# Kernel tuning notes

Measured on AMD Instinct MI355X. Metric: run time of the kernel, lower is better.

## Reference

```python
import jax, jax.numpy as jnp
import numpy as np

HEAD_DIM = 128
N_HEADS = 32
ROPE_DIM = 64
TOPK = 1024
B, S, HID, QLORA = 1, 2048, 4096, 1536
LN_EPS = 1e-5  # torch nn.LayerNorm default


def _hadamard_matrix(n):
    H = np.array([[1.0]], dtype=np.float32)
    while H.shape[0] < n:
        H = np.block([[H, H], [H, -H]])
    return jnp.asarray(H)

_H128 = _hadamard_matrix(HEAD_DIM)
_FWHT_SCALE = HEAD_DIM ** -0.5


def rotate_activation(x):
    # Fast Walsh-Hadamard transform == x @ H_sylvester, scaled by dim**-0.5
    return (x @ _H128) * _FWHT_SCALE


def rope_non_interleaved(x, cos, sin):
    # x: [..., rope_dim]; cos/sin: broadcastable [..., rope_dim/2]
    half = x.shape[-1] // 2
    x1, x2 = x[..., :half], x[..., half:]
    return jnp.concatenate([x1 * cos - x2 * sin, x1 * sin + x2 * cos], axis=-1)


def setup_inputs() -> dict:
    key = jax.random.key(0)
    ks = jax.random.split(key, 8)
    hidden_states = jax.random.normal(ks[0], (B, S, HID), jnp.float32)
    q_compressed = jax.random.normal(ks[1], (B, S, QLORA), jnp.float32)
    # rotary cos/sin for rope_dim=64 (standard concat layout)
    pos = jnp.arange(S, dtype=jnp.float32)
    inv_freq = 1.0 / (10000.0 ** (jnp.arange(0, ROPE_DIM, 2, dtype=jnp.float32) / ROPE_DIM))
    ang = pos[:, None] * inv_freq[None, :]  # [S, 32]
    cos = jnp.tile(jnp.cos(ang), (1, 2))[None]  # [1, S, 64]
    sin = jnp.tile(jnp.sin(ang), (1, 2))[None]
    # additive causal mask [B, S, S]
    causal = jnp.tril(jnp.ones((S, S), jnp.bool_))
    attention_mask = jnp.where(causal, 0.0, -1e9).astype(jnp.float32)[None]
    Wq_b = jax.random.normal(ks[2], (QLORA, N_HEADS * HEAD_DIM), jnp.float32) * (QLORA ** -0.5)
    Wk = jax.random.normal(ks[3], (HID, HEAD_DIM), jnp.float32) * (HID ** -0.5)
    k_gamma = jnp.ones((HEAD_DIM,), jnp.float32)
    k_beta = jnp.zeros((HEAD_DIM,), jnp.float32)
    Ww = jax.random.normal(ks[4], (HID, N_HEADS), jnp.float32) * (HID ** -0.5)
    return {"hidden_states": hidden_states, "q_compressed": q_compressed, "cos": cos,
            "sin": sin, "attention_mask": attention_mask, "Wq_b": Wq_b, "Wk": Wk,
            "k_gamma": k_gamma, "k_beta": k_beta, "Ww": Ww}


def reference(hidden_states, q_compressed, cos, sin, attention_mask, Wq_b, Wk, k_gamma, k_beta, Ww):
    b, s, _ = hidden_states.shape
    softmax_scale = HEAD_DIM ** -0.5
    # queries: [b, s, H, D]
    q = (q_compressed @ Wq_b).reshape(b, s, N_HEADS, HEAD_DIM)
    q_rope, q_nope = q[..., :ROPE_DIM], q[..., ROPE_DIM:]
    # keys: single shared head, LayerNorm(k)
    k = hidden_states @ Wk  # [b, s, D]
    mu = jnp.mean(k, axis=-1, keepdims=True)
    var = jnp.mean(jnp.square(k - mu), axis=-1, keepdims=True)
    k = (k - mu) * jax.lax.rsqrt(var + LN_EPS) * k_gamma + k_beta
    k_rope, k_nope = k[..., :ROPE_DIM], k[..., ROPE_DIM:]
    # non-interleaved RoPE (cos/sin truncated to half_dim=32)
    half = ROPE_DIM // 2
    c, sn = cos[..., :half], sin[..., :half]
    q_rope = rope_non_interleaved(q_rope, c[:, :, None, :], sn[:, :, None, :])
    k_rope = rope_non_interleaved(k_rope, c, sn)
    q = jnp.concatenate([q_rope, q_nope], axis=-1)
    k = jnp.concatenate([k_rope, k_nope], axis=-1)
    # Hadamard activation rotation
    q = rotate_activation(q)
    k = rotate_activation(k)
    # I_{t,s} = sum_h w_{t,h} * ReLU(q_{t,h} . k_s) * scale
    scores = jax.nn.relu(jnp.einsum('bthd,bsd->bths', q, k)) * softmax_scale
    weights = hidden_states @ Ww  # [b, t, H]
    index_scores = jnp.einsum('bths,bth->bts', scores, weights)
    index_scores = index_scores + attention_mask
    topk = min(TOPK, s)
    _, topk_indices = jax.lax.top_k(index_scores, topk)  # [b, s, topk]
    return topk_indices, index_scores
```

## Files before the change

### kernel.cpp

```cpp
#include <hip/hip_runtime.h>
#include <stdint.h>

#define S_LEN 2048
#define HID 4096
#define QLORA 1536
#define NH 32
#define HD 128
#define TOPK_N 1024
#define NEG_INF -1000000000.0f
#define INV_SQRT_HD 0.08838834764831844f

typedef __attribute__((ext_vector_type(8))) short short8;
typedef __attribute__((ext_vector_type(4))) short short4_;
typedef __attribute__((ext_vector_type(4))) float float4_;
typedef __attribute__((ext_vector_type(4))) unsigned uint4_;
typedef __attribute__((ext_vector_type(4))) int int4_;
typedef __attribute__((ext_vector_type(2))) int int2_;

__device__ __forceinline__ short f2bf(float x) {
  union { float f; unsigned u; } v; v.f = x;
  unsigned r = v.u + 0x7FFFu + ((v.u >> 16) & 1u);
  return (short)(r >> 16);
}

__device__ __forceinline__ unsigned f2ord(float x) {
  union { float f; unsigned u; } v; v.f = x;
  return v.u ^ (0x80000000u | (unsigned)((int)v.u >> 31));
}

__device__ __forceinline__ void gload_lds16(const void* g, void* l) {
  __builtin_amdgcn_global_load_lds((const __attribute__((address_space(1))) unsigned int*)g,
                                   (__attribute__((address_space(3))) unsigned int*)l, 16, 0, 0);
}

__global__ __launch_bounds__(256) void prep_kernel(
    const float* __restrict__ hidden, short* __restrict__ hidb,
    const float* __restrict__ qc, char* __restrict__ qc8,
    float* __restrict__ kacc,
    const float* __restrict__ wqb, char* __restrict__ wq8T,
    const float* __restrict__ wk, const float* __restrict__ ww,
    short* __restrict__ kwT) {
  __shared__ __align__(8) char stile[4352];
  int bid = blockIdx.x;
  const int tid = threadIdx.x;
  if (bid < 8192) {
    int i = bid * 256 + tid;
    float4 v = ((const float4*)hidden)[i];
    short4_ o;
    o[0] = f2bf(v.x); o[1] = f2bf(v.y); o[2] = f2bf(v.z); o[3] = f2bf(v.w);
    ((short4_*)hidb)[i] = o;
    return;
  }
  if (bid < 9728) {
    int i = (bid - 8192) * 256 + tid;
    float4 f0 = ((const float4*)qc)[i * 2];
    float4 f1 = ((const float4*)qc)[i * 2 + 1];
    int lo = 0, hi = 0;
    lo = __builtin_amdgcn_cvt_pk_fp8_f32(f0.x, f0.y, lo, 0);
    lo = __builtin_amdgcn_cvt_pk_fp8_f32(f0.z, f0.w, lo, 1);
    hi = __builtin_amdgcn_cvt_pk_fp8_f32(f1.x, f1.y, hi, 0);
    hi = __builtin_amdgcn_cvt_pk_fp8_f32(f1.z, f1.w, hi, 1);
    ((int2_*)qc8)[i] = (int2_){lo, hi};
    return;
  }
  if (bid < 10048) {
    int i = (bid - 9728) * 256 + tid;
    ((float4_*)kacc)[i] = (float4_){0.f, 0.f, 0.f, 0.f};
    return;
  }
  if (bid < 13120) {
    char (*t8)[33] = (char(*)[33])stile;
    int b = bid - 10048;
    int k0 = (b >> 7) * 64, n0 = (b & 127) * 32;
    #pragma unroll
    for (int i = 0; i < 8; i++) {
      int e = tid + i * 256;
      int r = e >> 5, c = e & 31;
      float x = wqb[(size_t)(k0 + r) * HID + n0 + c];
      t8[r][c] = (char)__builtin_amdgcn_cvt_pk_fp8_f32(x, x, 0, 0);
    }
    __syncthreads();
    int nl = tid >> 3, jk = (tid & 7) * 8;
    union { char c[8]; long l; } o;
    #pragma unroll
    for (int j = 0; j < 8; j++) o.c[j] = t8[jk + j][nl];
    *(long*)(wq8T + (size_t)(n0 + nl) * QLORA + k0 + jk) = o.l;
    return;
  }
  short (*tile)[33] = (short(*)[33])stile;
  const float* in; short* out; int R, C, bx, by;
  if (bid < 13632) {
    int b2 = bid - 13120;
    in = wk; out = kwT; R = HID; C = HD; bx = b2 & 3; by = b2 >> 2;
  } else {
    int b3 = bid - 13632;
    in = ww; out = kwT + 128 * HID; R = HID; C = NH; bx = 0; by = b3;
  }
  int c0 = bx * 32, r0 = by * 32;
  int tx = tid & 31, ty = tid >> 5;
  #pragma unroll
  for (int i = 0; i < 32; i += 8)
    tile[ty + i][tx] = f2bf(in[(size_t)(r0 + ty + i) * C + c0 + tx]);
  __syncthreads();
  #pragma unroll
  for (int i = 0; i < 32; i += 8)
    out[(size_t)(c0 + ty + i) * R + r0 + tx] = tile[tx][ty + i];
}

#define QSTAGE8(kt, Ad, Bd) do { \
  _Pragma("unroll") \
  for (int i = 0; i < 4; i++) { \
    int m = w * 32 + i * 8 + lr; \
    int gb = (kt) * 128 + ((lc ^ (m & 7)) << 4); \
    gload_lds16(qc8 + (size_t)(t0 + m) * QLORA + gb, (Ad) + (w * 32 + i * 8) * 128); \
    gload_lds16(wq8T + (size_t)(n0 + m) * QLORA + gb, (Bd) + (w * 32 + i * 8) * 128); \
  } \
} while (0)

#define QCOMPUTE8(Aq, Bq) do { \
  _Pragma("unroll") \
  for (int p = 0; p < 4; p++) { \
    int ch = p * 2 + (quad >> 1); \
    int lo8 = (quad & 1) * 8; \
    long a[2], b[8]; \
    _Pragma("unroll") \
    for (int mt = 0; mt < 2; mt++) { \
      int m = w * 32 + mt * 16 + l15; \
      a[mt] = *(const long*)((Aq) + m * 128 + ((ch ^ (m & 7)) << 4) + lo8); \
    } \
    _Pragma("unroll") \
    for (int nt = 0; nt < 8; nt++) { \
      int n = nt * 16 + l15; \
      b[nt] = *(const long*)((Bq) + n * 128 + ((ch ^ (n & 7)) << 4) + lo8); \
    } \
    _Pragma("unroll") \
    for (int mt = 0; mt < 2; mt++) \
      _Pragma("unroll") \
      for (int nt = 0; nt < 8; nt++) \
        acc[mt][nt] = __builtin_amdgcn_mfma_f32_16x16x32_fp8_fp8(a[mt], b[nt], acc[mt][nt], 0, 0, 0); \
  } \
} while (0)

__global__ __launch_bounds__(256, 2) void gemms_kernel(
    const char* __restrict__ qc8, const char* __restrict__ wq8T,
    const float* __restrict__ cosp, const float* __restrict__ sinp,
    short* __restrict__ qrot,
    const short* __restrict__ hidb, const short* __restrict__ kwT,
    float* __restrict__ kacc) {
  __shared__ __align__(16) char smem[65536];
  const int tid = threadIdx.x;
  const int w = tid >> 6, lane = tid & 63;
  const int l15 = lane & 15, quad = lane >> 4;
  const int lr = lane >> 3, lc = lane & 7;

  if (blockIdx.x < 512) {
    char* A0 = smem;
    char* B0 = smem + 16384;
    char* A1 = smem + 32768;
    char* B1 = smem + 49152;
    const int n0 = (blockIdx.x & 31) * 128;
    const int t0 = (blockIdx.x >> 5) * 128;

    float4_ acc[2][8];
    #pragma unroll
    for (int mt = 0; mt < 2; mt++)
      #pragma unroll
      for (int i = 0; i < 8; i++) acc[mt][i] = (float4_){0.f, 0.f, 0.f, 0.f};

    QSTAGE8(0, A0, B0);
    __syncthreads();
    for (int kt = 0; kt < 12; kt += 2) {
      QSTAGE8(kt + 1, A1, B1);
      QCOMPUTE8(A0, B0);
      __syncthreads();
      if (kt + 2 < 12) QSTAGE8(kt + 2, A0, B0);
      QCOMPUTE8(A1, B1);
      __syncthreads();
    }

    #pragma unroll
    for (int mt = 0; mt < 2; mt++) {
      #pragma unroll
      for (int r = 0; r < 4; r++) {
        const int trow = t0 + w * 32 + mt * 16 + quad * 4 + r;
        float v[8];
        #pragma unroll
        for (int nt = 0; nt < 8; nt++) v[nt] = acc[mt][nt][r];
        float cc0 = cosp[trow * 64 + l15], cc1 = cosp[trow * 64 + 16 + l15];
        float ss0 = sinp[trow * 64 + l15], ss1 = sinp[trow * 64 + 16 + l15];
        float r0 = v[0] * cc0 - v[2] * ss0, r1 = v[1] * cc1 - v[3] * ss1;
        float r2 = v[0] * ss0 + v[2] * cc0, r3 = v[1] * ss1 + v[3] * cc1;
        v[0] = r0; v[1] = r1; v[2] = r2; v[3] = r3;
        short* orow = qrot + (size_t)trow * HID + n0;
        #pragma unroll
        for (int nt = 0; nt < 8; nt++)
          orow[nt * 16 + l15] = f2bf(v[nt]);
      }
    }
  } else {
    short* Al = (short*)smem;
    short* Bl = (short*)(smem + 8192);
    const int b2 = blockIdx.x - 512;
    const int kc0 = (b2 & 7) * 512;
    const int m0g = (b2 >> 3) * 64;

    float4_ acc[10];
    #pragma unroll
    for (int i = 0; i < 10; i++) acc[i] = (float4_){0.f, 0.f, 0.f, 0.f};

    for (int k0 = kc0; k0 < kc0 + 512; k0 += 64) {
      #pragma unroll
      for (int i = 0; i < 2; i++) {
        int m = w * 16 + i * 8 + lr;
        int gk = k0 + ((lc ^ (m & 7)) << 3);
        gload_lds16(hidb + (size_t)(m0g + m) * HID + gk, Al + (w * 16 + i * 8) * 64);
      }
      #pragma unroll
      for (int i = 0; i < 5; i++) {
        int n = w * 40 + i * 8 + lr;
        int gk = k0 + ((lc ^ (n & 7)) << 3);
        gload_lds16(kwT + (size_t)n * HID + gk, Bl + (w * 40 + i * 8) * 64);
      }
      __syncthreads();
      #pragma unroll
      for (int kk = 0; kk < 64; kk += 32) {
        int ca = (kk >> 3) + quad;
        int ma = w * 16 + l15;
        short8 a = *(const short8*)(Al + ma * 64 + ((ca ^ (ma & 7)) << 3));
        #pragma unroll
        for (int nt = 0; nt < 10; nt++) {
          int n = nt * 16 + l15;
          short8 b = *(const short8*)(Bl + n * 64 + ((ca ^ (n & 7)) << 3));
          acc[nt] = __builtin_amdgcn_mfma_f32_16x16x32_bf16(a, b, acc[nt], 0, 0, 0);
        }
      }
      __syncthreads();
    }
    #pragma unroll
    for (int nt = 0; nt < 10; nt++)
      #pragma unroll
      for (int r = 0; r < 4; r++) {
        int row = m0g + w * 16 + quad * 4 + r;
        atomicAdd(&kacc[(size_t)row * 160 + nt * 16 + l15], acc[nt][r]);
      }
  }
}

__global__ __launch_bounds__(256) void ln_rope_kernel(
    const float* __restrict__ kacc, const float* __restrict__ gamma,
    const float* __restrict__ beta, const float* __restrict__ cosp,
    const float* __restrict__ sinp, short* __restrict__ krot) {
  const int tid = threadIdx.x;
  const int row = blockIdx.x * 16 + (tid >> 4);
  const int l16 = tid & 15;
  const int c0 = l16 * 8;
  const float* rp = kacc + (size_t)row * 160 + c0;
  float4 f0 = ((const float4*)rp)[0], f1 = ((const float4*)rp)[1];
  float v[8] = {f0.x, f0.y, f0.z, f0.w, f1.x, f1.y, f1.z, f1.w};
  float s = 0.f, ss = 0.f;
  #pragma unroll
  for (int j = 0; j < 8; j++) { s += v[j]; ss += v[j] * v[j]; }
  #pragma unroll
  for (int d = 1; d <= 8; d <<= 1) {
    s += __shfl_xor(s, d, 64); ss += __shfl_xor(ss, d, 64);
  }
  float mu = s * (1.0f / 128.0f);
  float var = ss * (1.0f / 128.0f) - mu * mu;
  float rs = rsqrtf(var + 1e-5f);
  #pragma unroll
  for (int j = 0; j < 8; j++)
    v[j] = (v[j] - mu) * rs * gamma[c0 + j] + beta[c0 + j];
  #pragma unroll
  for (int j = 0; j < 8; j++) {
    float p = __shfl_xor(v[j], 4, 64);
    if (l16 < 8) {
      int idx = (c0 + j) & 31;
      float c = cosp[row * 64 + idx], sn = sinp[row * 64 + idx];
      v[j] = v[j] * c + p * ((l16 < 4) ? -sn : sn);
    }
  }
  short8 o;
  #pragma unroll
  for (int j = 0; j < 8; j++) o[j] = f2bf(v[j]);
  *(short8*)(krot + (size_t)row * 128 + c0) = o;
}

__global__ __launch_bounds__(256, 2) void scores_kernel(
    const short* __restrict__ qrot, const short* __restrict__ krot,
    const float* __restrict__ kacc, float* __restrict__ isc) {
  __shared__ __align__(16) char smem[65536];
  short* buf0 = (short*)smem;
  short* buf1 = (short*)(smem + 32768);

  const int tid = threadIdx.x;
  const int w = tid >> 6, lane = tid & 63;
  const int l15 = lane & 15, quad = lane >> 4;
  const int wm = w >> 1, wn = w & 1;
  const int lr16 = lane >> 4, lc16 = lane & 15;

  const int bid = blockIdx.x;
  const int strip = (bid & 1) ? (511 - (bid >> 1)) : (bid >> 1);
  const int t0 = strip * 4;
  const int nsb = (t0 + 3) / 128 + 1;

  const short* Abase = qrot + (size_t)t0 * 32 * 128;
  #pragma unroll
  for (int i = 0; i < 8; i++) {
    int m = (w * 8 + i) * 4 + lr16;
    int gofs = m * 128 + ((lc16 ^ (m & 7)) << 3);
    gload_lds16(Abase + gofs, buf0 + (w * 8 + i) * 512);
    gload_lds16(krot + gofs, buf1 + (w * 8 + i) * 512);
  }
  __syncthreads();

  short8 af[4][4];
  #pragma unroll
  for (int k4 = 0; k4 < 4; k4++) {
    int ca = k4 * 4 + quad;
    #pragma unroll
    for (int mt = 0; mt < 4; mt++) {
      int m = wm * 64 + mt * 16 + l15;
      af[k4][mt] = *(const short8*)(buf0 + m * 128 + ((ca ^ (m & 7)) << 3));
    }
  }

  const int t_a = t0 + wm * 2, t_b = t_a + 1;
  float wq[4][4];
  #pragma unroll
  for (int mt = 0; mt < 4; mt++) {
    int tt = (mt < 2) ? t_a : t_b;
    #pragma unroll
    for (int r = 0; r < 4; r++)
      wq[mt][r] = kacc[(size_t)tt * 160 + 128 + (mt & 1) * 16 + quad * 4 + r];
  }
  __syncthreads();

  for (int sb = 0; sb < nsb; sb++) {
    short* cur = (sb & 1) ? buf0 : buf1;
    if (sb + 1 < nsb) {
      short* nxt = (sb & 1) ? buf1 : buf0;
      const short* Bbase = krot + (size_t)(sb + 1) * 128 * 128;
      #pragma unroll
      for (int i = 0; i < 8; i++) {
        int m = (w * 8 + i) * 4 + lr16;
        int gofs = m * 128 + ((lc16 ^ (m & 7)) << 3);
        gload_lds16(Bbase + gofs, nxt + (w * 8 + i) * 512);
      }
    }

    float4_ acc[4][4];
    #pragma unroll
    for (int mt = 0; mt < 4; mt++)
      #pragma unroll
      for (int nt = 0; nt < 4; nt++) acc[mt][nt] = (float4_){0.f, 0.f, 0.f, 0.f};

    #pragma unroll
    for (int k4 = 0; k4 < 4; k4++) {
      int ca = k4 * 4 + quad;
      short8 b[4];
      #pragma unroll
      for (int nt = 0; nt < 4; nt++) {
        int n = wn * 64 + nt * 16 + l15;
        b[nt] = *(const short8*)(cur + n * 128 + ((ca ^ (n & 7)) << 3));
      }
      #pragma unroll
      for (int mt = 0; mt < 4; mt++)
        #pragma unroll
        for (int nt = 0; nt < 4; nt++)
          acc[mt][nt] = __builtin_amdgcn_mfma_f32_16x16x32_bf16(af[k4][mt], b[nt], acc[mt][nt], 0, 0, 0);
    }

    #pragma unroll
    for (int nt = 0; nt < 4; nt++) {
      float pa = 0.f, pb = 0.f;
      #pragma unroll
      for (int r = 0; r < 4; r++) {
        pa += fmaxf(acc[0][nt][r], 0.f) * wq[0][r] + fmaxf(acc[1][nt][r], 0.f) * wq[1][r];
        pb += fmaxf(acc[2][nt][r], 0.f) * wq[2][r] + fmaxf(acc[3][nt][r], 0.f) * wq[3][r];
      }
      pa += __shfl_xor(pa, 16, 64); pa += __shfl_xor(pa, 32, 64);
      pb += __shfl_xor(pb, 16, 64); pb += __shfl_xor(pb, 32, 64);
      int s = sb * 128 + wn * 64 + nt * 16 + l15;
      if (quad == 0)
        isc[(size_t)t_a * S_LEN + s] = (s <= t_a) ? pa * INV_SQRT_HD : NEG_INF;
      else if (quad == 1)
        isc[(size_t)t_b * S_LEN + s] = (s <= t_b) ? pb * INV_SQRT_HD : NEG_INF;
    }

    __syncthreads();
  }

  if (wn == 0) {
    const int myrow = (lane < 32) ? t_a : t_b;
    const int l32 = lane & 31;
    float4_ nf = (float4_){NEG_INF, NEG_INF, NEG_INF, NEG_INF};
    float4_* rowp = (float4_*)(isc + (size_t)myrow * S_LEN);
    for (int i = nsb * 32 + l32; i < 512; i += 32) rowp[i] = nf;
  }
}

#define CEK(x, y, d) { if ((d) ? (v[x] < v[y]) : (v[x] > v[y])) { unsigned _t = v[x]; v[x] = v[y]; v[y] = _t; } }

__device__ __forceinline__ void shfl_phase(unsigned v[8], int j, int base, bool d) {
  const int delta = j >> 3;
  const bool keep_max = (((base & j) == 0) == d);
  #pragma unroll
  for (int r = 0; r < 8; r++) {
    unsigned pv = (unsigned)__shfl_xor((int)v[r], delta, 64);
    unsigned mx = v[r] > pv ? v[r] : pv;
    unsigned mn = v[r] > pv ? pv : v[r];
    v[r] = keep_max ? mx : mn;
  }
}

__device__ __forceinline__ void reg_phase(unsigned v[8], bool d) {
  CEK(0, 4, d); CEK(1, 5, d); CEK(2, 6, d); CEK(3, 7, d);
  CEK(0, 2, d); CEK(1, 3, d); CEK(4, 6, d); CEK(5, 7, d);
  CEK(0, 1, d); CEK(2, 3, d); CEK(4, 5, d); CEK(6, 7, d);
}

__device__ __forceinline__ int chswz(int c) { return c ^ ((c >> 3) & 7); }

__device__ __forceinline__ void lds_phase(unsigned v[8], unsigned* keys, int tid, int base,
                                          int j, bool d) {
  const int c0 = tid * 2, c1 = c0 + 1;
  ((uint4_*)keys)[chswz(c0)] = (uint4_){v[0], v[1], v[2], v[3]};
  ((uint4_*)keys)[chswz(c1)] = (uint4_){v[4], v[5], v[6], v[7]};
  __syncthreads();
  const int ptid = tid ^ (j >> 3);
  uint4_ u0 = ((uint4_*)keys)[chswz(ptid * 2)];
  uint4_ u1 = ((uint4_*)keys)[chswz(ptid * 2 + 1)];
  unsigned p[8] = {u0[0], u0[1], u0[2], u0[3], u1[0], u1[1], u1[2], u1[3]};
  const bool keep_max = (((base & j) == 0) == d);
  #pragma unroll
  for (int r = 0; r < 8; r++) {
    unsigned mx = v[r] > p[r] ? v[r] : p[r];
    unsigned mn = v[r] > p[r] ? p[r] : v[r];
    v[r] = keep_max ? mx : mn;
  }
  __syncthreads();
}

__global__ __launch_bounds__(256) void topk_kernel(const float* __restrict__ isc,
                                                   int* __restrict__ idx_out) {
  __shared__ __align__(16) unsigned keys[2048];
  const int t = blockIdx.x;
  const int tid = threadIdx.x;
  const int base = tid * 8;
  unsigned v[8];
  {
    const float* row = isc + (size_t)t * S_LEN;
    float4 f0 = ((const float4*)row)[tid * 2];
    float4 f1 = ((const float4*)row)[tid * 2 + 1];
    v[0] = (f2ord(f0.x) & 0xFFFFF800u) | (unsigned)(2047 - base - 0);
    v[1] = (f2ord(f0.y) & 0xFFFFF800u) | (unsigned)(2047 - base - 1);
    v[2] = (f2ord(f0.z) & 0xFFFFF800u) | (unsigned)(2047 - base - 2);
    v[3] = (f2ord(f0.w) & 0xFFFFF800u) | (unsigned)(2047 - base - 3);
    v[4] = (f2ord(f1.x) & 0xFFFFF800u) | (unsigned)(2047 - base - 4);
    v[5] = (f2ord(f1.y) & 0xFFFFF800u) | (unsigned)(2047 - base - 5);
    v[6] = (f2ord(f1.z) & 0xFFFFF800u) | (unsigned)(2047 - base - 6);
    v[7] = (f2ord(f1.w) & 0xFFFFF800u) | (unsigned)(2047 - base - 7);
  }
  CEK(0, 1, true); CEK(2, 3, false); CEK(4, 5, true); CEK(6, 7, false);
  CEK(0, 2, true); CEK(1, 3, true); CEK(4, 6, false); CEK(5, 7, false);
  CEK(0, 1, true); CEK(2, 3, true); CEK(4, 5, false); CEK(6, 7, false);
  {
    bool d8 = ((base & 8) == 0);
    CEK(0, 4, d8); CEK(1, 5, d8); CEK(2, 6, d8); CEK(3, 7, d8);
    CEK(0, 2, d8); CEK(1, 3, d8); CEK(4, 6, d8); CEK(5, 7, d8);
    CEK(0, 1, d8); CEK(2, 3, d8); CEK(4, 5, d8); CEK(6, 7, d8);
  }
  #pragma unroll
  for (int kb = 4; kb <= 11; kb++) {
    const int k = 1 << kb;
    const bool d = ((base & k) == 0);
    for (int j = k >> 1; j >= 512; j >>= 1)
      lds_phase(v, keys, tid, base, j, d);
    {
      int jtop = (k >> 1) < 256 ? (k >> 1) : 256;
      for (int j = jtop; j >= 8; j >>= 1)
        shfl_phase(v, j, base, d);
    }
    reg_phase(v, d);
  }
  if (tid < 128) {
    int4_ o0, o1;
    #pragma unroll
    for (int r = 0; r < 4; r++) o0[r] = 2047 - (int)(v[r] & 0x7FFu);
    #pragma unroll
    for (int r = 0; r < 4; r++) o1[r] = 2047 - (int)(v[4 + r] & 0x7FFu);
    ((int4_*)(idx_out + (size_t)t * TOPK_N))[tid * 2] = o0;
    ((int4_*)(idx_out + (size_t)t * TOPK_N))[tid * 2 + 1] = o1;
  }
}

extern "C" void kernel_launch(void* const* d_in, const int* in_sizes, int n_in,
                              void* d_out, int out_size, void* d_ws, size_t ws_size,
                              hipStream_t stream) {
  const float* hidden = (const float*)d_in[0];
  const float* qc     = (const float*)d_in[1];
  const float* cosp   = (const float*)d_in[2];
  const float* sinp   = (const float*)d_in[3];
  const float* wqb    = (const float*)d_in[5];
  const float* wk     = (const float*)d_in[6];
  const float* gamma  = (const float*)d_in[7];
  const float* beta   = (const float*)d_in[8];
  const float* ww     = (const float*)d_in[9];

  char* ws = (char*)d_ws;
  short* hidb = (short*)ws;
  char*  qc8  = (char*)(ws + 16777216);
  char*  wq8T = (char*)(ws + 19922944);
  short* kwT  = (short*)(ws + 26214400);
  short* krot = (short*)(ws + 27525120);
  short* qrot = (short*)(ws + 28049408);
  float* kacc = (float*)(ws + 44826624);

  int*   idx_out = (int*)d_out;
  float* isc     = ((float*)d_out) + (size_t)S_LEN * TOPK_N;

  prep_kernel<<<dim3(13760), dim3(256), 0, stream>>>(hidden, hidb, qc, qc8, kacc,
                                                     wqb, wq8T, wk, ww, kwT);
  gemms_kernel<<<dim3(768), dim3(256), 0, stream>>>(qc8, wq8T, cosp, sinp, qrot,
                                                    hidb, kwT, kacc);
  ln_rope_kernel<<<dim3(128), dim3(256), 0, stream>>>(kacc, gamma, beta, cosp, sinp, krot);
  scores_kernel<<<dim3(512), dim3(256), 0, stream>>>(qrot, krot, kacc, isc);
  topk_kernel<<<dim3(2048), dim3(256), 0, stream>>>(isc, idx_out);
}
```

Before: 246.1 us.

## Sort each top-k row within one wavefront using register bitonic networks

New measurement: 228.9 us. 7.0% less time.

```diff
diff --git a/kernel.cpp b/kernel.cpp
--- a/kernel.cpp
+++ b/kernel.cpp
@@ -399,98 +399,152 @@
   }
 }
 
-#define CEK(x, y, d) { if ((d) ? (v[x] < v[y]) : (v[x] > v[y])) { unsigned _t = v[x]; v[x] = v[y]; v[y] = _t; } }
-
-__device__ __forceinline__ void shfl_phase(unsigned v[8], int j, int base, bool d) {
-  const int delta = j >> 3;
-  const bool keep_max = (((base & j) == 0) == d);
-  #pragma unroll
-  for (int r = 0; r < 8; r++) {
-    unsigned pv = (unsigned)__shfl_xor((int)v[r], delta, 64);
-    unsigned mx = v[r] > pv ? v[r] : pv;
-    unsigned mn = v[r] > pv ? pv : v[r];
-    v[r] = keep_max ? mx : mn;
-  }
-}
-
-__device__ __forceinline__ void reg_phase(unsigned v[8], bool d) {
-  CEK(0, 4, d); CEK(1, 5, d); CEK(2, 6, d); CEK(3, 7, d);
-  CEK(0, 2, d); CEK(1, 3, d); CEK(4, 6, d); CEK(5, 7, d);
-  CEK(0, 1, d); CEK(2, 3, d); CEK(4, 5, d); CEK(6, 7, d);
-}
-
-__device__ __forceinline__ int chswz(int c) { return c ^ ((c >> 3) & 7); }
-
-__device__ __forceinline__ void lds_phase(unsigned v[8], unsigned* keys, int tid, int base,
-                                          int j, bool d) {
-  const int c0 = tid * 2, c1 = c0 + 1;
-  ((uint4_*)keys)[chswz(c0)] = (uint4_){v[0], v[1], v[2], v[3]};
-  ((uint4_*)keys)[chswz(c1)] = (uint4_){v[4], v[5], v[6], v[7]};
-  __syncthreads();
-  const int ptid = tid ^ (j >> 3);
-  uint4_ u0 = ((uint4_*)keys)[chswz(ptid * 2)];
-  uint4_ u1 = ((uint4_*)keys)[chswz(ptid * 2 + 1)];
-  unsigned p[8] = {u0[0], u0[1], u0[2], u0[3], u1[0], u1[1], u1[2], u1[3]};
-  const bool keep_max = (((base & j) == 0) == d);
-  #pragma unroll
-  for (int r = 0; r < 8; r++) {
-    unsigned mx = v[r] > p[r] ? v[r] : p[r];
-    unsigned mn = v[r] > p[r] ? p[r] : v[r];
-    v[r] = keep_max ? mx : mn;
-  }
-  __syncthreads();
-}
+
+__device__ __forceinline__ void ce(unsigned &a, unsigned &b, bool d) {
+  unsigned mx = a > b ? a : b;
+  unsigned mn = a > b ? b : a;
+  a = d ? mx : mn;
+  b = d ? mn : mx;
+}
+
+__device__ __forceinline__ void mtop3(unsigned* v, bool d) {
+  #pragma unroll
+  for (int j = 16; j >= 4; j >>= 1)
+    #pragma unroll
+    for (int r = 0; r < 32; ++r)
+      if (!(r & j)) ce(v[r], v[r ^ j], d);
+}
+
+template <int JT>
+__device__ __forceinline__ void mreg(unsigned* v, bool d) {
+  #pragma unroll
+  for (int j = JT; j >= 1; j >>= 1)
+    #pragma unroll
+    for (int r = 0; r < 32; ++r)
+      if (!(r & j)) ce(v[r], v[r ^ j], d);
+}
+
+#define IDX_L0   ((l << 5) | (q << 2))
+#define IDX_654  (((l >> 2) << 7) | (q << 4) | ((l & 3) << 2))
+#define IDX_765  (((l >> 3) << 8) | (q << 5) | ((l & 7) << 2))
+#define IDX_876  (((l >> 4) << 9) | (q << 6) | ((l & 15) << 2))
+#define IDX_543  (((l >> 1) << 6) | (q << 3) | ((l & 1) << 2))
+#define IDX_987  (((l >> 5) << 10) | (q << 7) | ((l & 31) << 2))
+#define IDX_1098 ((q << 8) | (l << 2))
+#define SWZW(ix) ((ix) ^ ((((ix) >> 5) & 7) << 2))
+
+#define RT(FROM, TO) do {                                               \
+  _Pragma("unroll")                                                     \
+  for (int q = 0; q < 8; ++q) {                                         \
+    int ix = (FROM);                                                    \
+    *(uint4_*)(buf + SWZW(ix)) =                                        \
+        (uint4_){v[4 * q], v[4 * q + 1], v[4 * q + 2], v[4 * q + 3]};   \
+  }                                                                     \
+  _Pragma("unroll")                                                     \
+  for (int q = 0; q < 8; ++q) {                                         \
+    int ix = (TO);                                                      \
+    uint4_ u = *(const uint4_*)(buf + SWZW(ix));                        \
+    v[4 * q] = u[0]; v[4 * q + 1] = u[1];                               \
+    v[4 * q + 2] = u[2]; v[4 * q + 3] = u[3];                           \
+  }                                                                     \
+} while (0)
 
 __global__ __launch_bounds__(256) void topk_kernel(const float* __restrict__ isc,
                                                    int* __restrict__ idx_out) {
-  __shared__ __align__(16) unsigned keys[2048];
-  const int t = blockIdx.x;
+  __shared__ __align__(16) unsigned sbuf[4][2048];
   const int tid = threadIdx.x;
-  const int base = tid * 8;
-  unsigned v[8];
+  const int w = tid >> 6, l = tid & 63;
+  unsigned* buf = sbuf[w];
+  const int gid = blockIdx.x * 4 + w;
+  const bool shortrow = (gid < 512);
+  int trow, sbase;
+  if (shortrow) { trow = gid * 2 + (l >> 5); sbase = (l & 31) << 5; }
+  else          { trow = 512 + gid;          sbase = l << 5; }
+
+  unsigned v[32];
   {
-    const float* row = isc + (size_t)t * S_LEN;
-    float4 f0 = ((const float4*)row)[tid * 2];
-    float4 f1 = ((const float4*)row)[tid * 2 + 1];
-    v[0] = (f2ord(f0.x) & 0xFFFFF800u) | (unsigned)(2047 - base - 0);
-    v[1] = (f2ord(f0.y) & 0xFFFFF800u) | (unsigned)(2047 - base - 1);
-    v[2] = (f2ord(f0.z) & 0xFFFFF800u) | (unsigned)(2047 - base - 2);
-    v[3] = (f2ord(f0.w) & 0xFFFFF800u) | (unsigned)(2047 - base - 3);
-    v[4] = (f2ord(f1.x) & 0xFFFFF800u) | (unsigned)(2047 - base - 4);
-    v[5] = (f2ord(f1.y) & 0xFFFFF800u) | (unsigned)(2047 - base - 5);
-    v[6] = (f2ord(f1.z) & 0xFFFFF800u) | (unsigned)(2047 - base - 6);
-    v[7] = (f2ord(f1.w) & 0xFFFFF800u) | (unsigned)(2047 - base - 7);
-  }
-  CEK(0, 1, true); CEK(2, 3, false); CEK(4, 5, true); CEK(6, 7, false);
-  CEK(0, 2, true); CEK(1, 3, true); CEK(4, 6, false); CEK(5, 7, false);
-  CEK(0, 1, true); CEK(2, 3, true); CEK(4, 5, false); CEK(6, 7, false);
+    const float* rp = isc + (size_t)trow * S_LEN + sbase;
+    #pragma unroll
+    for (int g = 0; g < 8; ++g) {
+      float4 f = ((const float4*)rp)[g];
+      unsigned b0 = (unsigned)(2047 - (sbase + g * 4));
+      v[g * 4 + 0] = (f2ord(f.x) & 0xFFFFF800u) | b0;
+      v[g * 4 + 1] = (f2ord(f.y) & 0xFFFFF800u) | (b0 - 1);
+      v[g * 4 + 2] = (f2ord(f.z) & 0xFFFFF800u) | (b0 - 2);
+      v[g * 4 + 3] = (f2ord(f.w) & 0xFFFFF800u) | (b0 - 3);
+    }
+  }
+
+  #pragma unroll
+  for (int r = 0; r < 32; r += 2) ce(v[r], v[r + 1], ((r & 2) == 0));
+  #pragma unroll
+  for (int j = 2; j >= 1; j >>= 1)
+    #pragma unroll
+    for (int r = 0; r < 32; ++r)
+      if (!(r & j)) ce(v[r], v[r ^ j], ((r & 4) == 0));
+  #pragma unroll
+  for (int j = 4; j >= 1; j >>= 1)
+    #pragma unroll
+    for (int r = 0; r < 32; ++r)
+      if (!(r & j)) ce(v[r], v[r ^ j], ((r & 8) == 0));
+  #pragma unroll
+  for (int j = 8; j >= 1; j >>= 1)
+    #pragma unroll
+    for (int r = 0; r < 32; ++r)
+      if (!(r & j)) ce(v[r], v[r ^ j], ((r & 16) == 0));
+
+  mreg<16>(v, (l & 1) == 0);
+
   {
-    bool d8 = ((base & 8) == 0);
-    CEK(0, 4, d8); CEK(1, 5, d8); CEK(2, 6, d8); CEK(3, 7, d8);
-    CEK(0, 2, d8); CEK(1, 3, d8); CEK(4, 6, d8); CEK(5, 7, d8);
-    CEK(0, 1, d8); CEK(2, 3, d8); CEK(4, 5, d8); CEK(6, 7, d8);
-  }
-  #pragma unroll
-  for (int kb = 4; kb <= 11; kb++) {
-    const int k = 1 << kb;
-    const bool d = ((base & k) == 0);
-    for (int j = k >> 1; j >= 512; j >>= 1)
-      lds_phase(v, keys, tid, base, j, d);
-    {
-      int jtop = (k >> 1) < 256 ? (k >> 1) : 256;
-      for (int j = jtop; j >= 8; j >>= 1)
-        shfl_phase(v, j, base, d);
-    }
-    reg_phase(v, d);
-  }
-  if (tid < 128) {
-    int4_ o0, o1;
-    #pragma unroll
-    for (int r = 0; r < 4; r++) o0[r] = 2047 - (int)(v[r] & 0x7FFu);
-    #pragma unroll
-    for (int r = 0; r < 4; r++) o1[r] = 2047 - (int)(v[4 + r] & 0x7FFu);
-    ((int4_*)(idx_out + (size_t)t * TOPK_N))[tid * 2] = o0;
-    ((int4_*)(idx_out + (size_t)t * TOPK_N))[tid * 2 + 1] = o1;
+    bool d = ((l & 2) == 0);
+    bool keep = (((l & 1) == 0) == d);
+    #pragma unroll
+    for (int r = 0; r < 32; ++r) {
+      unsigned pv = (unsigned)__shfl_xor((int)v[r], 1, 64);
+      unsigned mx = v[r] > pv ? v[r] : pv;
+      unsigned mn = v[r] > pv ? pv : v[r];
+      v[r] = keep ? mx : mn;
+    }
+    mreg<16>(v, d);
+  }
+
+  {
+    bool d = ((l & 4) == 0);
+    RT(IDX_L0, IDX_654);  mtop3(v, d);
+    RT(IDX_654, IDX_L0);  mreg<8>(v, d);
+  }
+  {
+    bool d = ((l & 8) == 0);
+    RT(IDX_L0, IDX_765);  mtop3(v, d);
+    RT(IDX_765, IDX_L0);  mreg<16>(v, d);
+  }
+  {
+    bool d = ((l & 16) == 0);
+    RT(IDX_L0, IDX_876);  mtop3(v, d);
+    RT(IDX_876, IDX_543); mtop3(v, d);
+    RT(IDX_543, IDX_L0);  mreg<4>(v, d);
+  }
+  {
+    bool d = shortrow ? true : (l < 32);
+    RT(IDX_L0, IDX_987);  mtop3(v, d);
+    RT(IDX_987, IDX_654); mtop3(v, d);
+    RT(IDX_654, IDX_L0);  mreg<8>(v, d);
+  }
+  if (!shortrow) {
+    RT(IDX_L0, IDX_1098); mtop3(v, true);
+    RT(IDX_1098, IDX_765); mtop3(v, true);
+    RT(IDX_765, IDX_L0);  mreg<16>(v, true);
+  }
+
+  if (shortrow || l < 32) {
+    int* op = idx_out + (size_t)trow * TOPK_N + sbase;
+    #pragma unroll
+    for (int g = 0; g < 8; ++g) {
+      int4_ o;
+      #pragma unroll
+      for (int j = 0; j < 4; ++j) o[j] = 2047 - (int)(v[g * 4 + j] & 0x7FFu);
+      ((int4_*)op)[g] = o;
+    }
   }
 }
 
@@ -525,5 +579,5 @@
                                                     hidb, kwT, kacc);
   ln_rope_kernel<<<dim3(128), dim3(256), 0, stream>>>(kacc, gamma, beta, cosp, sinp, krot);
   scores_kernel<<<dim3(512), dim3(256), 0, stream>>>(qrot, krot, kacc, isc);
-  topk_kernel<<<dim3(2048), dim3(256), 0, stream>>>(isc, idx_out);
-}
+  topk_kernel<<<dim3(384), dim3(256), 0, stream>>>(isc, idx_out);
+}
```
